# Kernel optimization log

Measured on AMD Instinct MI355X. Metric: run time of the kernel, lower is better.

## Reference

```python
import jax, jax.numpy as jnp
import numpy as np
from jax import lax

B, R, C_FEAT, HF, WF = 4, 512, 256, 50, 50
NUM_CLASSES = 91
POOL = 7
SCALE = 1.0 / 16.0
IMG_H = IMG_W = 800.0
SCORE_THRESH = 0.05
NMS_THRESH = 0.5
DETS_PER_IMG = 100
TOPK_NMS = 2048  # fixed-size candidate set for static-shape NMS
BBOX_W = np.array([10.0, 10.0, 5.0, 5.0], np.float32)
BBOX_CLIP = float(np.log(1000.0 / 16.0))
MIN_SIZE = 0.01


def setup_inputs():
    key = jax.random.key(0)
    ks = jax.random.split(key, 8)
    features = jax.random.normal(ks[0], (B, C_FEAT, HF, WF), jnp.float32)
    cxy = jax.random.uniform(ks[1], (B, R, 2), jnp.float32, 50.0, 750.0)
    wh = jax.random.uniform(ks[2], (B, R, 2), jnp.float32, 20.0, 200.0)
    proposals = jnp.concatenate([cxy - wh / 2, cxy + wh / 2], axis=-1)
    d_in = C_FEAT * POOL * POOL
    def lin(k, fi, fo):
        return jax.random.normal(k, (fi, fo), jnp.float32) / np.sqrt(fi)
    return {
        'features': features, 'proposals': proposals,
        'W1': lin(ks[3], d_in, 1024), 'b1': jnp.zeros((1024,), jnp.float32),
        'W2': lin(ks[4], 1024, 1024), 'b2': jnp.zeros((1024,), jnp.float32),
        'Wc': lin(ks[5], 1024, NUM_CLASSES), 'bc': jnp.zeros((NUM_CLASSES,), jnp.float32),
        'Wr': lin(ks[6], 1024, 4 * NUM_CLASSES), 'br': jnp.zeros((4 * NUM_CLASSES,), jnp.float32),
    }


def roi_align(features, proposals):
    # features [B,C,H,W], proposals [B,R,4] in image coords -> [B*R, C*POOL*POOL]
    featT = jnp.transpose(features, (0, 2, 3, 1))  # [B,H,W,C]
    boxes = proposals * SCALE
    x1, y1, x2, y2 = (boxes[..., i] for i in range(4))
    bh = (y2 - y1) / POOL
    bw = (x2 - x1) / POOL
    centers = jnp.arange(POOL, dtype=jnp.float32) + 0.5
    ys = y1[..., None] + centers * bh[..., None]  # [B,R,P]
    xs = x1[..., None] + centers * bw[..., None]  # [B,R,P]

    def bil(fT, ys_b, xs_b):  # per-image bilinear sampling
        yy = jnp.broadcast_to(ys_b[:, :, None], (R, POOL, POOL))
        xx = jnp.broadcast_to(xs_b[:, None, :], (R, POOL, POOL))
        y = jnp.clip(yy, 0.0, HF - 1.0)
        x = jnp.clip(xx, 0.0, WF - 1.0)
        y0 = jnp.floor(y); x0 = jnp.floor(x)
        y0i = y0.astype(jnp.int32); x0i = x0.astype(jnp.int32)
        y1i = jnp.minimum(y0i + 1, HF - 1); x1i = jnp.minimum(x0i + 1, WF - 1)
        ly = y - y0; lx = x - x0; hy = 1.0 - ly; hx = 1.0 - lx
        f00 = fT[y0i, x0i]; f01 = fT[y0i, x1i]
        f10 = fT[y1i, x0i]; f11 = fT[y1i, x1i]  # [R,P,P,C]
        out = ((hy * hx)[..., None] * f00 + (hy * lx)[..., None] * f01 +
               (ly * hx)[..., None] * f10 + (ly * lx)[..., None] * f11)
        return out  # [R,P,P,C]

    pooled = jax.vmap(bil)(featT, ys, xs)  # [B,R,P,P,C]
    pooled = jnp.transpose(pooled, (0, 1, 4, 2, 3))  # [B,R,C,P,P] (torch layout)
    return pooled.reshape(B * R, -1)


def decode_boxes(box_reg, props):
    # box_reg [N, 4*NC], props [N,4] -> [N,NC,4]
    w = props[:, 2] - props[:, 0]
    h = props[:, 3] - props[:, 1]
    cx = props[:, 0] + 0.5 * w
    cy = props[:, 1] + 0.5 * h
    d = box_reg.reshape(-1, NUM_CLASSES, 4) / jnp.asarray(BBOX_W)
    dx, dy = d[..., 0], d[..., 1]
    dw = jnp.minimum(d[..., 2], BBOX_CLIP)
    dh = jnp.minimum(d[..., 3], BBOX_CLIP)
    pcx = dx * w[:, None] + cx[:, None]
    pcy = dy * h[:, None] + cy[:, None]
    pw = jnp.exp(dw) * w[:, None]
    ph = jnp.exp(dh) * h[:, None]
    return jnp.stack([pcx - 0.5 * pw, pcy - 0.5 * ph,
                      pcx + 0.5 * pw, pcy + 0.5 * ph], axis=-1)


def box_iou(a, b):
    area_a = (a[:, 2] - a[:, 0]) * (a[:, 3] - a[:, 1])
    area_b = (b[:, 2] - b[:, 0]) * (b[:, 3] - b[:, 1])
    lt = jnp.maximum(a[:, None, :2], b[None, :, :2])
    rb = jnp.minimum(a[:, None, 2:], b[None, :, 2:])
    wh = jnp.clip(rb - lt, 0.0)
    inter = wh[..., 0] * wh[..., 1]
    return inter / (area_a[:, None] + area_b[None, :] - inter)


def post_image(boxes, scores):
    # boxes [R,NC,4], scores [R,NC] -> fixed-size top DETS_PER_IMG detections
    x1 = jnp.clip(boxes[..., 0], 0.0, IMG_W)
    y1 = jnp.clip(boxes[..., 1], 0.0, IMG_H)
    x2 = jnp.clip(boxes[..., 2], 0.0, IMG_W)
    y2 = jnp.clip(boxes[..., 3], 0.0, IMG_H)
    boxes = jnp.stack([x1, y1, x2, y2], axis=-1)
    # drop background class 0, flatten (roi, class) candidates
    boxes = boxes[:, 1:].reshape(-1, 4)            # [R*(NC-1),4]
    scores = scores[:, 1:].reshape(-1)
    labels = jnp.broadcast_to(jnp.arange(1, NUM_CLASSES, dtype=jnp.int32)[None, :],
                              (R, NUM_CLASSES - 1)).reshape(-1)
    wv = boxes[:, 2] - boxes[:, 0]
    hv = boxes[:, 3] - boxes[:, 1]
    valid = (scores > SCORE_THRESH) & (wv >= MIN_SIZE) & (hv >= MIN_SIZE)
    cand = jnp.where(valid, scores, -1.0)
    top_s, top_i = lax.top_k(cand, TOPK_NMS)       # sorted desc by score
    b_k = boxes[top_i]
    l_k = labels[top_i]
    v_k = valid[top_i]
    # batched (per-class) NMS via label offset
    off = l_k.astype(jnp.float32)[:, None] * (IMG_W + 1.0)
    iou = box_iou(b_k + off, b_k + off)            # [K,K]
    idx = jnp.arange(TOPK_NMS)

    def body(i, keep):
        sup = jnp.any((idx < i) & keep & (iou[:, i] > NMS_THRESH))
        return keep.at[i].set(keep[i] & ~sup)

    keep = lax.fori_loop(0, TOPK_NMS, body, v_k)
    fs = jnp.where(keep, top_s, -1.0)
    out_s, out_i = lax.top_k(fs, DETS_PER_IMG)
    ok = out_s > 0.0
    out_b = jnp.where(ok[:, None], b_k[out_i], 0.0)
    out_l = jnp.where(ok, l_k[out_i], 0)
    out_s = jnp.where(ok, out_s, 0.0)
    return out_b, out_s, out_l


def reference(features, proposals, W1, b1, W2, b2, Wc, bc, Wr, br):
    x = roi_align(features, proposals)               # [B*R, C*49]
    x = jax.nn.relu(x @ W1 + b1)
    x = jax.nn.relu(x @ W2 + b2)
    class_logits = x @ Wc + bc                        # [B*R, NC]
    box_regression = x @ Wr + br                      # [B*R, 4*NC]
    props_flat = proposals.reshape(-1, 4)
    pred_boxes = decode_boxes(box_regression, props_flat).reshape(B, R, NUM_CLASSES, 4)
    pred_scores = jax.nn.softmax(class_logits, axis=-1).reshape(B, R, NUM_CLASSES)
    boxes, scores, labels = jax.vmap(post_image)(pred_boxes, pred_scores)
    return boxes, scores, labels


if __name__ == '__main__':
    out = reference(**setup_inputs())
    print([o.shape for o in out])
```

## Files before the change

kernel.cpp:

```cpp
#include <hip/hip_runtime.h>
#include <stdint.h>

#define NBI 4
#define RRI 512
#define NROI 2048
#define DIN 12544
#define BBOX_CLIP_F 4.135166556742356f

typedef _Float16 half8 __attribute__((ext_vector_type(8)));
typedef float f32x16 __attribute__((ext_vector_type(16)));

#define O_AH      10240000ull
#define O_AL      61620224ull
#define O_WTH     113000448ull
#define O_WTL     138690560ull
#define OZ        164380672ull
#define WS_NEED   189546496ull

#define O_X2H     0ull
#define O_X2L     2097152ull
#define O_X1H     O_AH
#define O_X1L     (O_AH + 4194304ull)
#define O_PBOX    O_AL
#define O_KEYS    (O_AL + 2949120ull)
#define O_NMSBOX  (O_AL + 3473408ull)
#define O_OUTBOX  (O_AL + 3604480ull)
#define O_SCORE   (O_AL + 3735552ull)
#define O_LABEL   (O_AL + 3768320ull)
#define O_CNT     (O_AL + 3801088ull)
#define O_MASK    (O_AL + 3802112ull)
#define O_WHH     O_WTH
#define O_WHL     (O_WTH + 1048576ull)
#define O_BH      (O_WTH + 2097152ull)
#define O_PARTH   (O_WTH + 2101248ull)
#define O_HEADF   (O_WTH + 18878464ull)
#define O_W2TH    OZ
#define O_W2TL    (OZ + 2097152ull)
#define O_PFC2    (OZ + 4194304ull)

__global__ void k_zero_out(float* __restrict__ out) {
  int i = blockIdx.x * 256 + threadIdx.x;
  if (i < 2400) out[i] = 0.0f;
}

__global__ void k_zero2(unsigned* __restrict__ keys32, unsigned* __restrict__ cnt) {
  int i = blockIdx.x * 256 + threadIdx.x;
  if (i < 131072) keys32[i] = 0u;
  if (i < 64) cnt[i] = 0u;
}

__global__ __launch_bounds__(256) void k_transpose(const float* __restrict__ f,
                                                   float* __restrict__ ft) {
  __shared__ float s[32][33];
  int b = blockIdx.z;
  int hw0 = blockIdx.x << 5;
  int c0 = blockIdx.y << 5;
  int tx = threadIdx.x & 31, ty = threadIdx.x >> 5;
#pragma unroll
  for (int j = 0; j < 32; j += 8) {
    int hw = hw0 + tx;
    if (hw < 2500) s[ty + j][tx] = f[((size_t)b * 256 + c0 + ty + j) * 2500 + hw];
  }
  __syncthreads();
#pragma unroll
  for (int j = 0; j < 32; j += 8) {
    int hw = hw0 + ty + j;
    if (hw < 2500) ft[((size_t)b * 2500 + hw) * 256 + c0 + tx] = s[tx][ty + j];
  }
}

__global__ __launch_bounds__(256) void k_wsplit(const float* __restrict__ W,
                                                _Float16* __restrict__ Th,
                                                _Float16* __restrict__ Tl, int K, int N) {
  __shared__ float s[64][68];
  int k0 = blockIdx.x << 6, n0 = blockIdx.y << 6;
  int t = threadIdx.x;
  int r = t >> 2, c4 = (t & 3) << 4;
#pragma unroll
  for (int j = 0; j < 16; j += 4) {
    float4 v = *(const float4*)(W + (size_t)(k0 + r) * N + n0 + c4 + j);
    s[r][c4 + j] = v.x; s[r][c4 + j + 1] = v.y; s[r][c4 + j + 2] = v.z; s[r][c4 + j + 3] = v.w;
  }
  __syncthreads();
  int nr = t >> 2, kc = (t & 3) << 4;
  half8 h8[2], l8[2];
#pragma unroll
  for (int j = 0; j < 16; ++j) {
    float v = s[kc + j][nr];
    _Float16 h = (_Float16)v;
    _Float16 lo = (_Float16)((v - (float)h) * 2048.0f);
    h8[j >> 3][j & 7] = h;
    l8[j >> 3][j & 7] = lo;
  }
  size_t base = (size_t)(n0 + nr) * K + k0 + kc;
  *(half8*)(Th + base) = h8[0]; *(half8*)(Th + base + 8) = h8[1];
  *(half8*)(Tl + base) = l8[0]; *(half8*)(Tl + base + 8) = l8[1];
}

__global__ __launch_bounds__(256) void k_wsplit_heads(const float* __restrict__ Wc,
                                                      const float* __restrict__ Wr,
                                                      const float* __restrict__ bcv,
                                                      const float* __restrict__ brv,
                                                      _Float16* __restrict__ Th,
                                                      _Float16* __restrict__ Tl,
                                                      float* __restrict__ bh) {
  int n = blockIdx.x;
  int t = threadIdx.x;
  for (int k = t; k < 1024; k += 256) {
    float v = (n < 91) ? Wc[(size_t)k * 91 + n]
                       : ((n < 455) ? Wr[(size_t)k * 364 + (n - 91)] : 0.0f);
    _Float16 h = (_Float16)v;
    Th[(size_t)n * 1024 + k] = h;
    Tl[(size_t)n * 1024 + k] = (_Float16)((v - (float)h) * 2048.0f);
  }
  if (t == 0) bh[n] = (n < 91) ? bcv[n] : ((n < 455) ? brv[n - 91] : 0.0f);
}

__global__ __launch_bounds__(256) void k_roialign(const float* __restrict__ ft,
                                                  const float* __restrict__ props,
                                                  _Float16* __restrict__ Ahg,
                                                  _Float16* __restrict__ Alg) {
  __shared__ float pool[DIN];
  __shared__ float lyA[7], lxA[7];
  __shared__ int y0A[7], y1A[7], x0A[7], x1A[7];
  int roi = blockIdx.x;
  int b = roi >> 9;
  const float* p = props + (size_t)roi * 4;
  float x1s = p[0] * 0.0625f, y1s = p[1] * 0.0625f;
  float x2s = p[2] * 0.0625f, y2s = p[3] * 0.0625f;
  float bh = (y2s - y1s) / 7.0f;
  float bw = (x2s - x1s) / 7.0f;
  int t = threadIdx.x;
  if (t < 7) {
    float y = y1s + ((float)t + 0.5f) * bh;
    y = fminf(fmaxf(y, 0.0f), 49.0f);
    float y0 = floorf(y);
    int y0i = (int)y0;
    y0A[t] = y0i; y1A[t] = min(y0i + 1, 49); lyA[t] = y - y0;
  } else if (t < 14) {
    int px = t - 7;
    float x = x1s + ((float)px + 0.5f) * bw;
    x = fminf(fmaxf(x, 0.0f), 49.0f);
    float x0 = floorf(x);
    int x0i = (int)x0;
    x0A[px] = x0i; x1A[px] = min(x0i + 1, 49); lxA[px] = x - x0;
  }
  __syncthreads();
  const float* fb = ft + (size_t)b * 2500 * 256;
  int c = t;
  for (int p49 = 0; p49 < 49; ++p49) {
    int py = p49 / 7, px = p49 - py * 7;
    int y0 = y0A[py], y1 = y1A[py], x0 = x0A[px], x1 = x1A[px];
    float ly = lyA[py], lx = lxA[px], hy = 1.0f - ly, hx = 1.0f - lx;
    float f00 = fb[(y0 * 50 + x0) * 256 + c];
    float f01 = fb[(y0 * 50 + x1) * 256 + c];
    float f10 = fb[(y1 * 50 + x0) * 256 + c];
    float f11 = fb[(y1 * 50 + x1) * 256 + c];
    pool[c * 49 + p49] = (hy * hx) * f00 + (hy * lx) * f01 + (ly * hx) * f10 + (ly * lx) * f11;
  }
  __syncthreads();
  _Float16* dh = Ahg + (size_t)roi * DIN;
  _Float16* dl = Alg + (size_t)roi * DIN;
  for (int i = t; i < DIN; i += 256) {
    float v = pool[i];
    _Float16 h = (_Float16)v;
    dh[i] = h;
    dl[i] = (_Float16)((v - (float)h) * 2048.0f);
  }
}

__global__ __launch_bounds__(256, 2) void k_mfma(const _Float16* __restrict__ Ah,
                                                 const _Float16* __restrict__ Al,
                                                 const _Float16* __restrict__ Bh,
                                                 const _Float16* __restrict__ Bl,
                                                 float* __restrict__ P0,
                                                 float* __restrict__ P2,
                                                 int K, int K2, int ldc, int MN) {
  __shared__ __align__(16) _Float16 sA[2][128][32];
  __shared__ __align__(16) _Float16 sB[2][128][32];
  int gx = gridDim.x, gy = gridDim.y;
  int nwg = gx * gy * gridDim.z;
  int lin = blockIdx.x + gx * (blockIdx.y + gy * blockIdx.z);
  int cpx = nwg >> 3;
  int nl = (lin & 7) * cpx + (lin >> 3);
  int sx = __ffs(gx) - 1, sy = __ffs(gy) - 1;
  int lx = nl & (gx - 1);
  int rest = nl >> sx;
  int ly = rest & (gy - 1);
  int lz = rest >> sy;
  int m0 = ly << 7, n0 = lx << 7;
  int kb = lz * K2;
  int t = threadIdx.x;
  int w = t >> 6, l = t & 63;
  int wr = w >> 1, wc = w & 1;
  int srow = t >> 1, sh = t & 1;
  const _Float16* gAh = Ah + (size_t)(m0 + srow) * K + kb + sh * 16;
  const _Float16* gAl = Al + (size_t)(m0 + srow) * K + kb + sh * 16;
  const _Float16* gBh = Bh + (size_t)(n0 + srow) * K + kb + sh * 16;
  const _Float16* gBl = Bl + (size_t)(n0 + srow) * K + kb + sh * 16;
  int rsw = (srow >> 1) & 3;
  int wof0 = ((2 * sh) ^ rsw) << 3;
  int wof1 = ((2 * sh + 1) ^ rsw) << 3;
  f32x16 accH[2][2], accL[2][2];
#pragma unroll
  for (int i = 0; i < 2; ++i)
#pragma unroll
    for (int j = 0; j < 2; ++j)
#pragma unroll
      for (int r = 0; r < 16; ++r) { accH[i][j][r] = 0.0f; accL[i][j][r] = 0.0f; }
  half8 pAh0 = *(const half8*)gAh, pAh1 = *(const half8*)(gAh + 8);
  half8 pAl0 = *(const half8*)gAl, pAl1 = *(const half8*)(gAl + 8);
  half8 pBh0 = *(const half8*)gBh, pBh1 = *(const half8*)(gBh + 8);
  half8 pBl0 = *(const half8*)gBl, pBl1 = *(const half8*)(gBl + 8);
  int fr = l & 31, cgrp = l >> 5;
  for (int kt = 0; kt < K2; kt += 32) {
    __syncthreads();
    *(half8*)&sA[0][srow][wof0] = pAh0;
    *(half8*)&sA[0][srow][wof1] = pAh1;
    *(half8*)&sA[1][srow][wof0] = pAl0;
    *(half8*)&sA[1][srow][wof1] = pAl1;
    *(half8*)&sB[0][srow][wof0] = pBh0;
    *(half8*)&sB[0][srow][wof1] = pBh1;
    *(half8*)&sB[1][srow][wof0] = pBl0;
    *(half8*)&sB[1][srow][wof1] = pBl1;
    __syncthreads();
    if (kt + 32 < K2) {
      pAh0 = *(const half8*)(gAh + kt + 32); pAh1 = *(const half8*)(gAh + kt + 40);
      pAl0 = *(const half8*)(gAl + kt + 32); pAl1 = *(const half8*)(gAl + kt + 40);
      pBh0 = *(const half8*)(gBh + kt + 32); pBh1 = *(const half8*)(gBh + kt + 40);
      pBl0 = *(const half8*)(gBl + kt + 32); pBl1 = *(const half8*)(gBl + kt + 40);
    }
#pragma unroll
    for (int s = 0; s < 2; ++s) {
      int c2 = s * 2 + cgrp;
      half8 aH[2], aL[2], bH[2], bL[2];
#pragma unroll
      for (int mf = 0; mf < 2; ++mf) {
        int row = wr * 64 + mf * 32 + fr;
        int co = (c2 ^ ((row >> 1) & 3)) << 3;
        aH[mf] = *(const half8*)&sA[0][row][co];
        aL[mf] = *(const half8*)&sA[1][row][co];
      }
#pragma unroll
      for (int nf = 0; nf < 2; ++nf) {
        int row = wc * 64 + nf * 32 + fr;
        int co = (c2 ^ ((row >> 1) & 3)) << 3;
        bH[nf] = *(const half8*)&sB[0][row][co];
        bL[nf] = *(const half8*)&sB[1][row][co];
      }
#pragma unroll
      for (int mf = 0; mf < 2; ++mf)
#pragma unroll
        for (int nf = 0; nf < 2; ++nf) {
          accH[mf][nf] =
              __builtin_amdgcn_mfma_f32_32x32x16_f16(aH[mf], bH[nf], accH[mf][nf], 0, 0, 0);
          accL[mf][nf] =
              __builtin_amdgcn_mfma_f32_32x32x16_f16(aH[mf], bL[nf], accL[mf][nf], 0, 0, 0);
          accL[mf][nf] =
              __builtin_amdgcn_mfma_f32_32x32x16_f16(aL[mf], bH[nf], accL[mf][nf], 0, 0, 0);
        }
    }
  }
  float* Pz = (lz == 2) ? P2 : (P0 + (size_t)(lz == 3 ? 2 : lz) * MN);
  const float sc = 4.8828125e-4f;
#pragma unroll
  for (int mf = 0; mf < 2; ++mf)
#pragma unroll
    for (int nf = 0; nf < 2; ++nf) {
      int col = n0 + wc * 64 + nf * 32 + fr;
      int rbase = m0 + wr * 64 + mf * 32 + 4 * cgrp;
#pragma unroll
      for (int r = 0; r < 16; ++r) {
        int row = rbase + (r & 3) + ((r >> 2) << 3);
        Pz[(size_t)row * ldc + col] = accH[mf][nf][r] + accL[mf][nf][r] * sc;
      }
    }
}

__global__ void k_reduce_split(const float* __restrict__ P0, const float* __restrict__ P2,
                               const float* __restrict__ bias, _Float16* __restrict__ xh,
                               _Float16* __restrict__ xl, int S) {
  const int MN = 2048 * 1024;
  int i8 = blockIdx.x * 256 + threadIdx.x;
  size_t base = (size_t)i8 * 8;
  float v[8];
  {
    float4 a0 = *(const float4*)(P0 + base);
    float4 a1 = *(const float4*)(P0 + base + 4);
    float4 b0 = *(const float4*)(P0 + MN + base);
    float4 b1 = *(const float4*)(P0 + MN + base + 4);
    v[0] = a0.x + b0.x; v[1] = a0.y + b0.y; v[2] = a0.z + b0.z; v[3] = a0.w + b0.w;
    v[4] = a1.x + b1.x; v[5] = a1.y + b1.y; v[6] = a1.z + b1.z; v[7] = a1.w + b1.w;
  }
  if (S == 4) {
    float4 c0 = *(const float4*)(P2 + base);
    float4 c1 = *(const float4*)(P2 + base + 4);
    float4 d0 = *(const float4*)(P0 + 2 * (size_t)MN + base);
    float4 d1 = *(const float4*)(P0 + 2 * (size_t)MN + base + 4);
    v[0] = (v[0] + c0.x) + d0.x; v[1] = (v[1] + c0.y) + d0.y;
    v[2] = (v[2] + c0.z) + d0.z; v[3] = (v[3] + c0.w) + d0.w;
    v[4] = (v[4] + c1.x) + d1.x; v[5] = (v[5] + c1.y) + d1.y;
    v[6] = (v[6] + c1.z) + d1.z; v[7] = (v[7] + c1.w) + d1.w;
  }
  int cb = (int)(base & 1023);
  float4 b0 = *(const float4*)(bias + cb);
  float4 b1v = *(const float4*)(bias + cb + 4);
  v[0] += b0.x; v[1] += b0.y; v[2] += b0.z; v[3] += b0.w;
  v[4] += b1v.x; v[5] += b1v.y; v[6] += b1v.z; v[7] += b1v.w;
  half8 h8, l8;
#pragma unroll
  for (int j = 0; j < 8; ++j) {
    float x = fmaxf(v[j], 0.0f);
    _Float16 h = (_Float16)x;
    h8[j] = h;
    l8[j] = (_Float16)((x - (float)h) * 2048.0f);
  }
  *(half8*)(xh + base) = h8;
  *(half8*)(xl + base) = l8;
}

__global__ void k_headreduce(const float4* __restrict__ PH, const float* __restrict__ bh,
                             float4* __restrict__ head) {
  const int MN4 = 2048 * 512 / 4;
  int i = blockIdx.x * 256 + threadIdx.x;
  float4 p0 = PH[i], p1 = PH[i + MN4], p2 = PH[i + 3 * MN4], p3 = PH[i + 2 * MN4];
  const float4 b = *(const float4*)(bh + ((i & 127) << 2));
  float4 o;
  o.x = ((p0.x + p1.x) + p2.x) + p3.x + b.x;
  o.y = ((p0.y + p1.y) + p2.y) + p3.y + b.y;
  o.z = ((p0.z + p1.z) + p2.z) + p3.z + b.z;
  o.w = ((p0.w + p1.w) + p2.w) + p3.w + b.w;
  head[i] = o;
}

__global__ __launch_bounds__(256) void k_softmax_decode(const float* __restrict__ head,
                                                        const float* __restrict__ props,
                                                        float* __restrict__ pbox,
                                                        unsigned long long* __restrict__ keys,
                                                        unsigned* __restrict__ cnt) {
  int wave = threadIdx.x >> 6, lane = threadIdx.x & 63;
  int roi = (blockIdx.x << 2) + wave;
  const float* hr = head + (size_t)roi * 512;
  float l0 = hr[lane];
  float l1 = (lane < 27) ? hr[lane + 64] : -3.4e38f;
  float m = fmaxf(l0, l1);
#pragma unroll
  for (int off = 32; off; off >>= 1) m = fmaxf(m, __shfl_xor(m, off));
  float e0 = expf(l0 - m);
  float e1 = (lane < 27) ? expf(l1 - m) : 0.0f;
  float ssum = e0 + e1;
#pragma unroll
  for (int off = 32; off; off >>= 1) ssum += __shfl_xor(ssum, off);
  const float* pr = props + (size_t)roi * 4;
  float w = pr[2] - pr[0], h = pr[3] - pr[1];
  float cx = pr[0] + 0.5f * w, cy = pr[1] + 0.5f * h;
  int img = roi >> 9, rl = roi & 511;
#pragma unroll
  for (int half = 0; half < 2; ++half) {
    int c = lane + half * 64;
    float e = half ? e1 : e0;
    if (c >= 1 && c <= 90) {
      float score = e / ssum;
      const float* rg = hr + 91 + (c << 2);
      float dx = rg[0] / 10.0f, dy = rg[1] / 10.0f;
      float dw = fminf(rg[2] / 5.0f, BBOX_CLIP_F);
      float dh = fminf(rg[3] / 5.0f, BBOX_CLIP_F);
      float pcx = dx * w + cx, pcy = dy * h + cy;
      float pw = expf(dw) * w, ph = expf(dh) * h;
      float bx1 = pcx - 0.5f * pw, by1 = pcy - 0.5f * ph;
      float bx2 = pcx + 0.5f * pw, by2 = pcy + 0.5f * ph;
      bx1 = fminf(fmaxf(bx1, 0.0f), 800.0f);
      by1 = fminf(fmaxf(by1, 0.0f), 800.0f);
      bx2 = fminf(fmaxf(bx2, 0.0f), 800.0f);
      by2 = fminf(fmaxf(by2, 0.0f), 800.0f);
      float* pb = pbox + ((size_t)roi * 90 + (c - 1)) * 4;
      pb[0] = bx1; pb[1] = by1; pb[2] = bx2; pb[3] = by2;
      if (score > 0.05f && (bx2 - bx1) >= 0.01f && (by2 - by1) >= 0.01f) {
        unsigned pos = atomicAdd(cnt + img, 1u);
        unsigned idx = (unsigned)rl * 90u + (unsigned)(c - 1);
        unsigned su = __float_as_uint(score);
        su ^= (su >> 31) ? 0xFFFFFFFFu : 0x80000000u;
        keys[((size_t)img << 14) + pos] =
            ((unsigned long long)su << 32) | (unsigned long long)(0xFFFFFFFFu - idx);
      }
    }
  }
}

__global__ void k_sort(unsigned long long* __restrict__ keys, const unsigned* __restrict__ cnt) {
  extern __shared__ unsigned long long s[];
  int img = blockIdx.x, tid = threadIdx.x;
  unsigned long long* kb = keys + ((size_t)img << 14);
  unsigned n = cnt[img];
  unsigned np = 2048; while (np < n && np < 16384) np <<= 1;
  if (np <= 8192) {
    for (unsigned i = tid; i < np; i += 1024) s[i] = kb[i];
    __syncthreads();
    for (unsigned k = 2; k <= np; k <<= 1) {
      for (unsigned j = k >> 1; j; j >>= 1) {
        for (unsigned x = tid; x < (np >> 1); x += 1024) {
          unsigned i = ((x & ~(j - 1)) << 1) | (x & (j - 1));
          unsigned l = i | j;
          bool up = ((i & k) == 0);
          unsigned long long a = s[i], b = s[l];
          if ((a > b) == up) { s[i] = b; s[l] = a; }
        }
        __syncthreads();
      }
    }
    for (unsigned i = tid; i < np; i += 1024) kb[i] = s[i];
  } else {
    for (int ch = 0; ch < 2; ++ch) {
      unsigned base = (unsigned)ch << 13;
      for (unsigned i = tid; i < 8192; i += 1024) s[i] = kb[base + i];
      __syncthreads();
      for (unsigned k = 2; k <= 8192; k <<= 1) {
        for (unsigned j = k >> 1; j; j >>= 1) {
          for (unsigned x = tid; x < 4096; x += 1024) {
            unsigned i = ((x & ~(j - 1)) << 1) | (x & (j - 1));
            unsigned l = i | j;
            bool up = (((base + i) & k) == 0);
            unsigned long long a = s[i], b = s[l];
            if ((a > b) == up) { s[i] = b; s[l] = a; }
          }
          __syncthreads();
        }
      }
      for (unsigned i = tid; i < 8192; i += 1024) kb[base + i] = s[i];
      __syncthreads();
    }
    for (unsigned x = tid; x < 8192; x += 1024) {
      unsigned long long a = kb[x], b = kb[x + 8192];
      if (a > b) { kb[x] = b; kb[x + 8192] = a; }
    }
    __syncthreads();
    for (int ch = 0; ch < 2; ++ch) {
      unsigned base = (unsigned)ch << 13;
      for (unsigned i = tid; i < 8192; i += 1024) s[i] = kb[base + i];
      __syncthreads();
      for (unsigned j = 4096; j; j >>= 1) {
        for (unsigned x = tid; x < 4096; x += 1024) {
          unsigned i = ((x & ~(j - 1)) << 1) | (x & (j - 1));
          unsigned l = i | j;
          unsigned long long a = s[i], b = s[l];
          if (a > b) { s[i] = b; s[l] = a; }
        }
        __syncthreads();
      }
      for (unsigned i = tid; i < 8192; i += 1024) kb[base + i] = s[i];
      __syncthreads();
    }
  }
}

__global__ void k_gather(const unsigned long long* __restrict__ keys,
                         const unsigned* __restrict__ cnt, const float* __restrict__ pbox,
                         float4* __restrict__ nmsbox, float4* __restrict__ outbox,
                         float* __restrict__ score, float* __restrict__ label) {
  int g = blockIdx.x * 256 + threadIdx.x;
  int img = g >> 11, slot = g & 2047;
  unsigned n = cnt[img];
  unsigned neff = n > 2048u ? 2048u : n;
  unsigned np = 2048; while (np < n && np < 16384) np <<= 1;
  float4 bo = make_float4(0, 0, 0, 0), bx = make_float4(0, 0, 0, 0);
  float sc = -1.0f, lb = 0.0f;
  if ((unsigned)slot < neff) {
    unsigned long long key = keys[((size_t)img << 14) + (np - 1 - slot)];
    unsigned su = (unsigned)(key >> 32);
    su = (su & 0x80000000u) ? (su ^ 0x80000000u) : ~su;
    sc = __uint_as_float(su);
    unsigned idx = 0xFFFFFFFFu - (unsigned)(key & 0xFFFFFFFFull);
    unsigned rl = idx / 90u, c = idx - rl * 90u;
    const float* pb = pbox + ((size_t)((img << 9) + rl) * 90 + c) * 4;
    bx = *(const float4*)pb;
    float off = (float)(c + 1) * 801.0f;
    bo = make_float4(bx.x + off, bx.y + off, bx.z + off, bx.w + off);
    lb = (float)(c + 1);
  }
  nmsbox[g] = bo; outbox[g] = bx; score[g] = sc; label[g] = lb;
}

__global__ __launch_bounds__(256) void k_mask(const float* __restrict__ nmsbox,
                                              unsigned* __restrict__ mask) {
  __shared__ float bx[2048 * 4];
  int img = blockIdx.x >> 9;
  int i0 = (blockIdx.x & 511) << 2;
  const float4* src = (const float4*)(nmsbox + (size_t)img * 2048 * 4);
  for (int q = threadIdx.x; q < 2048; q += 256) ((float4*)bx)[q] = src[q];
  __syncthreads();
  int w = threadIdx.x & 63, ir = threadIdx.x >> 6;
  int i = i0 + ir;
  float ax1 = bx[i * 4], ay1 = bx[i * 4 + 1], ax2 = bx[i * 4 + 2], ay2 = bx[i * 4 + 3];
  float areaA = (ax2 - ax1) * (ay2 - ay1);
  unsigned bits = 0;
  for (int jj = 0; jj < 32; ++jj) {
    int j2 = (jj + w) & 31;
    int j = (w << 5) + j2;
    float b1 = bx[j * 4], b2 = bx[j * 4 + 1], b3 = bx[j * 4 + 2], b4 = bx[j * 4 + 3];
    float areaB = (b3 - b1) * (b4 - b2);
    float lx = fmaxf(ax1, b1), lyv = fmaxf(ay1, b2);
    float rx = fminf(ax2, b3), ry = fminf(ay2, b4);
    float iw = fmaxf(rx - lx, 0.0f), ih = fmaxf(ry - lyv, 0.0f);
    float inter = iw * ih;
    float iou = inter / (areaA + areaB - inter);
    if (iou > 0.5f) bits |= (1u << j2);
  }
  mask[((size_t)img * 2048 + i) * 64 + w] = bits;
}

__global__ void k_scan(const unsigned* __restrict__ mask, const unsigned* __restrict__ cnt,
                       const float* __restrict__ outbox, const float* __restrict__ score,
                       const float* __restrict__ label, float* __restrict__ dout) {
  int img = blockIdx.x, lane = threadIdx.x;
  unsigned n = cnt[img];
  unsigned neff = n > 2048u ? 2048u : n;
  unsigned base = (unsigned)lane * 32u;
  unsigned rem;
  if (base + 32u <= neff) rem = 0u;
  else if (base >= neff) rem = 0xFFFFFFFFu;
  else rem = ~((1u << (neff - base)) - 1u);
  const unsigned* mrow = mask + (size_t)img * 2048 * 64;
  unsigned row = (neff > 0) ? mrow[lane] : 0u;
  int outc = 0;
  for (int i = 0; i < (int)neff; ++i) {
    unsigned nextrow = (i + 1 < (int)neff) ? mrow[(size_t)(i + 1) * 64 + lane] : 0u;
    unsigned wrd = __shfl(rem, i >> 5);
    bool kept = ((wrd >> (i & 31)) & 1u) == 0u;
    if (kept) {
      rem |= row;
      if (lane < 4)
        dout[(size_t)(img * 100 + outc) * 4 + lane] = outbox[((size_t)img * 2048 + i) * 4 + lane];
      if (lane == 0) {
        dout[1600 + img * 100 + outc] = score[img * 2048 + i];
        dout[2000 + img * 100 + outc] = label[img * 2048 + i];
      }
      ++outc;
      if (outc >= 100) break;
    }
    row = nextrow;
  }
}

extern "C" void kernel_launch(void* const* d_in, const int* in_sizes, int n_in,
                              void* d_out, int out_size, void* d_ws, size_t ws_size,
                              hipStream_t stream) {
  if (ws_size < WS_NEED) return;

  const float* features  = (const float*)d_in[0];
  const float* proposals = (const float*)d_in[1];
  const float* W1 = (const float*)d_in[2];
  const float* b1 = (const float*)d_in[3];
  const float* W2 = (const float*)d_in[4];
  const float* b2 = (const float*)d_in[5];
  const float* Wc = (const float*)d_in[6];
  const float* bc = (const float*)d_in[7];
  const float* Wr = (const float*)d_in[8];
  const float* br = (const float*)d_in[9];
  float* out = (float*)d_out;
  char* ws = (char*)d_ws;

  float* featT = (float*)(ws + 0);
  _Float16* Ahg = (_Float16*)(ws + O_AH);
  _Float16* Alg = (_Float16*)(ws + O_AL);
  _Float16* Wth = (_Float16*)(ws + O_WTH);
  _Float16* Wtl = (_Float16*)(ws + O_WTL);
  float* partZ = (float*)(ws + OZ);
  float* partF = (float*)(ws + 0);
  _Float16* x1h = (_Float16*)(ws + O_X1H);
  _Float16* x1l = (_Float16*)(ws + O_X1L);
  _Float16* W2th = (_Float16*)(ws + O_W2TH);
  _Float16* W2tl = (_Float16*)(ws + O_W2TL);
  float* partC = (float*)(ws + O_PFC2);
  _Float16* x2h = (_Float16*)(ws + O_X2H);
  _Float16* x2l = (_Float16*)(ws + O_X2L);
  _Float16* whh = (_Float16*)(ws + O_WHH);
  _Float16* whl = (_Float16*)(ws + O_WHL);
  float* bhv   = (float*)(ws + O_BH);
  float* partH = (float*)(ws + O_PARTH);
  float* partH2 = (float*)(ws + O_PARTH + 3ull * 4194304ull);
  float* head  = (float*)(ws + O_HEADF);
  float* pbox  = (float*)(ws + O_PBOX);
  unsigned long long* keys = (unsigned long long*)(ws + O_KEYS);
  float* nmsbox = (float*)(ws + O_NMSBOX);
  float* outbox = (float*)(ws + O_OUTBOX);
  float* scorea = (float*)(ws + O_SCORE);
  float* labela = (float*)(ws + O_LABEL);
  unsigned* cnt = (unsigned*)(ws + O_CNT);
  unsigned* maska = (unsigned*)(ws + O_MASK);

  k_zero_out<<<10, 256, 0, stream>>>(out);
  k_transpose<<<dim3(79, 8, 4), 256, 0, stream>>>(features, featT);
  k_wsplit<<<dim3(196, 16), 256, 0, stream>>>(W1, Wth, Wtl, 12544, 1024);
  k_roialign<<<2048, 256, 0, stream>>>(featT, proposals, Ahg, Alg);
  k_mfma<<<dim3(8, 16, 4), 256, 0, stream>>>(Ahg, Alg, Wth, Wtl, partZ, partF,
                                             12544, 3136, 1024, 2048 * 1024);
  k_reduce_split<<<1024, 256, 0, stream>>>(partZ, partF, b1, x1h, x1l, 4);
  k_wsplit<<<dim3(16, 16), 256, 0, stream>>>(W2, W2th, W2tl, 1024, 1024);
  k_wsplit_heads<<<512, 256, 0, stream>>>(Wc, Wr, bc, br, whh, whl, bhv);
  k_mfma<<<dim3(8, 16, 2), 256, 0, stream>>>(x1h, x1l, W2th, W2tl, partC, partC,
                                             1024, 512, 1024, 2048 * 1024);
  k_reduce_split<<<1024, 256, 0, stream>>>(partC, partC, b2, x2h, x2l, 2);
  k_mfma<<<dim3(4, 16, 4), 256, 0, stream>>>(x2h, x2l, whh, whl, partH, partH2,
                                             1024, 256, 512, 2048 * 512);
  k_headreduce<<<1024, 256, 0, stream>>>((const float4*)partH, bhv, (float4*)head);
  k_zero2<<<512, 256, 0, stream>>>((unsigned*)keys, cnt);
  k_softmax_decode<<<512, 256, 0, stream>>>(head, proposals, pbox, keys, cnt);
  k_sort<<<4, 1024, 65536, stream>>>(keys, cnt);
  k_gather<<<32, 256, 0, stream>>>(keys, cnt, pbox, (float4*)nmsbox, (float4*)outbox,
                                   scorea, labela);
  k_mask<<<2048, 256, 0, stream>>>(nmsbox, maska);
  k_scan<<<4, 64, 0, stream>>>(maska, cnt, outbox, scorea, labela, out);
}
```

Before: 395.6 us.

## Load B fragments directly from global into registers and double-buffer A in LDS

The MFMA GEMM kernel no longer stages the B (weight) tile in shared memory. Each wave now loads its own B fragments straight from global memory into registers, prefetching the next k-slice while the current one computes. The A tile goes into a double-buffered LDS array, so each k-step needs one barrier instead of two. The aim is less LDS traffic and fewer barriers, at the cost of uncoalesced per-lane global reads of B (16 bytes per row) and more register pressure.

```diff
diff --git a/kernel.cpp b/kernel.cpp
--- a/kernel.cpp
+++ b/kernel.cpp
@@ -176,8 +176,7 @@
                                                  float* __restrict__ P0,
                                                  float* __restrict__ P2,
                                                  int K, int K2, int ldc, int MN) {
-  __shared__ __align__(16) _Float16 sA[2][128][32];
-  __shared__ __align__(16) _Float16 sB[2][128][32];
+  __shared__ __align__(16) _Float16 sA[2][2][128][32];
   int gx = gridDim.x, gy = gridDim.y;
   int nwg = gx * gy * gridDim.z;
   int lin = blockIdx.x + gx * (blockIdx.y + gy * blockIdx.z);
@@ -193,14 +192,17 @@
   int t = threadIdx.x;
   int w = t >> 6, l = t & 63;
   int wr = w >> 1, wc = w & 1;
+  int fr = l & 31, cgrp = l >> 5;
   int srow = t >> 1, sh = t & 1;
   const _Float16* gAh = Ah + (size_t)(m0 + srow) * K + kb + sh * 16;
   const _Float16* gAl = Al + (size_t)(m0 + srow) * K + kb + sh * 16;
-  const _Float16* gBh = Bh + (size_t)(n0 + srow) * K + kb + sh * 16;
-  const _Float16* gBl = Bl + (size_t)(n0 + srow) * K + kb + sh * 16;
   int rsw = (srow >> 1) & 3;
   int wof0 = ((2 * sh) ^ rsw) << 3;
   int wof1 = ((2 * sh + 1) ^ rsw) << 3;
+  const _Float16* pBh0 = Bh + (size_t)(n0 + wc * 64 + fr) * K + kb + cgrp * 8;
+  const _Float16* pBh1 = Bh + (size_t)(n0 + wc * 64 + 32 + fr) * K + kb + cgrp * 8;
+  const _Float16* pBl0 = Bl + (size_t)(n0 + wc * 64 + fr) * K + kb + cgrp * 8;
+  const _Float16* pBl1 = Bl + (size_t)(n0 + wc * 64 + 32 + fr) * K + kb + cgrp * 8;
   f32x16 accH[2][2], accL[2][2];
 #pragma unroll
   for (int i = 0; i < 2; ++i)
@@ -210,55 +212,70 @@
       for (int r = 0; r < 16; ++r) { accH[i][j][r] = 0.0f; accL[i][j][r] = 0.0f; }
   half8 pAh0 = *(const half8*)gAh, pAh1 = *(const half8*)(gAh + 8);
   half8 pAl0 = *(const half8*)gAl, pAl1 = *(const half8*)(gAl + 8);
-  half8 pBh0 = *(const half8*)gBh, pBh1 = *(const half8*)(gBh + 8);
-  half8 pBl0 = *(const half8*)gBl, pBl1 = *(const half8*)(gBl + 8);
-  int fr = l & 31, cgrp = l >> 5;
+  *(half8*)&sA[0][0][srow][wof0] = pAh0;
+  *(half8*)&sA[0][0][srow][wof1] = pAh1;
+  *(half8*)&sA[0][1][srow][wof0] = pAl0;
+  *(half8*)&sA[0][1][srow][wof1] = pAl1;
+  half8 cbh0 = *(const half8*)pBh0;
+  half8 cbh1 = *(const half8*)pBh1;
+  half8 cbl0 = *(const half8*)pBl0;
+  half8 cbl1 = *(const half8*)pBl1;
+  __syncthreads();
   for (int kt = 0; kt < K2; kt += 32) {
-    __syncthreads();
-    *(half8*)&sA[0][srow][wof0] = pAh0;
-    *(half8*)&sA[0][srow][wof1] = pAh1;
-    *(half8*)&sA[1][srow][wof0] = pAl0;
-    *(half8*)&sA[1][srow][wof1] = pAl1;
-    *(half8*)&sB[0][srow][wof0] = pBh0;
-    *(half8*)&sB[0][srow][wof1] = pBh1;
-    *(half8*)&sB[1][srow][wof0] = pBl0;
-    *(half8*)&sB[1][srow][wof1] = pBl1;
-    __syncthreads();
-    if (kt + 32 < K2) {
+    int buf = (kt >> 5) & 1;
+    bool more = (kt + 32) < K2;
+    if (more) {
       pAh0 = *(const half8*)(gAh + kt + 32); pAh1 = *(const half8*)(gAh + kt + 40);
       pAl0 = *(const half8*)(gAl + kt + 32); pAl1 = *(const half8*)(gAl + kt + 40);
-      pBh0 = *(const half8*)(gBh + kt + 32); pBh1 = *(const half8*)(gBh + kt + 40);
-      pBl0 = *(const half8*)(gBl + kt + 32); pBl1 = *(const half8*)(gBl + kt + 40);
-    }
-#pragma unroll
-    for (int s = 0; s < 2; ++s) {
-      int c2 = s * 2 + cgrp;
-      half8 aH[2], aL[2], bH[2], bL[2];
+    }
+    half8 nbh0 = *(const half8*)(pBh0 + kt + 16);
+    half8 nbh1 = *(const half8*)(pBh1 + kt + 16);
+    half8 nbl0 = *(const half8*)(pBl0 + kt + 16);
+    half8 nbl1 = *(const half8*)(pBl1 + kt + 16);
+    {
+      int c2 = cgrp;
 #pragma unroll
       for (int mf = 0; mf < 2; ++mf) {
         int row = wr * 64 + mf * 32 + fr;
         int co = (c2 ^ ((row >> 1) & 3)) << 3;
-        aH[mf] = *(const half8*)&sA[0][row][co];
-        aL[mf] = *(const half8*)&sA[1][row][co];
-      }
-#pragma unroll
-      for (int nf = 0; nf < 2; ++nf) {
-        int row = wc * 64 + nf * 32 + fr;
+        half8 aH = *(const half8*)&sA[buf][0][row][co];
+        half8 aL = *(const half8*)&sA[buf][1][row][co];
+        accH[mf][0] = __builtin_amdgcn_mfma_f32_32x32x16_f16(aH, cbh0, accH[mf][0], 0, 0, 0);
+        accL[mf][0] = __builtin_amdgcn_mfma_f32_32x32x16_f16(aH, cbl0, accL[mf][0], 0, 0, 0);
+        accL[mf][0] = __builtin_amdgcn_mfma_f32_32x32x16_f16(aL, cbh0, accL[mf][0], 0, 0, 0);
+        accH[mf][1] = __builtin_amdgcn_mfma_f32_32x32x16_f16(aH, cbh1, accH[mf][1], 0, 0, 0);
+        accL[mf][1] = __builtin_amdgcn_mfma_f32_32x32x16_f16(aH, cbl1, accL[mf][1], 0, 0, 0);
+        accL[mf][1] = __builtin_amdgcn_mfma_f32_32x32x16_f16(aL, cbh1, accL[mf][1], 0, 0, 0);
+      }
+    }
+    if (more) {
+      cbh0 = *(const half8*)(pBh0 + kt + 32);
+      cbh1 = *(const half8*)(pBh1 + kt + 32);
+      cbl0 = *(const half8*)(pBl0 + kt + 32);
+      cbl1 = *(const half8*)(pBl1 + kt + 32);
+    }
+    {
+      int c2 = 2 + cgrp;
+#pragma unroll
+      for (int mf = 0; mf < 2; ++mf) {
+        int row = wr * 64 + mf * 32 + fr;
         int co = (c2 ^ ((row >> 1) & 3)) << 3;
-        bH[nf] = *(const half8*)&sB[0][row][co];
-        bL[nf] = *(const half8*)&sB[1][row][co];
-      }
-#pragma unroll
-      for (int mf = 0; mf < 2; ++mf)
-#pragma unroll
-        for (int nf = 0; nf < 2; ++nf) {
-          accH[mf][nf] =
-              __builtin_amdgcn_mfma_f32_32x32x16_f16(aH[mf], bH[nf], accH[mf][nf], 0, 0, 0);
-          accL[mf][nf] =
-              __builtin_amdgcn_mfma_f32_32x32x16_f16(aH[mf], bL[nf], accL[mf][nf], 0, 0, 0);
-          accL[mf][nf] =
-              __builtin_amdgcn_mfma_f32_32x32x16_f16(aL[mf], bH[nf], accL[mf][nf], 0, 0, 0);
-        }
+        half8 aH = *(const half8*)&sA[buf][0][row][co];
+        half8 aL = *(const half8*)&sA[buf][1][row][co];
+        accH[mf][0] = __builtin_amdgcn_mfma_f32_32x32x16_f16(aH, nbh0, accH[mf][0], 0, 0, 0);
+        accL[mf][0] = __builtin_amdgcn_mfma_f32_32x32x16_f16(aH, nbl0, accL[mf][0], 0, 0, 0);
+        accL[mf][0] = __builtin_amdgcn_mfma_f32_32x32x16_f16(aL, nbh0, accL[mf][0], 0, 0, 0);
+        accH[mf][1] = __builtin_amdgcn_mfma_f32_32x32x16_f16(aH, nbh1, accH[mf][1], 0, 0, 0);
+        accL[mf][1] = __builtin_amdgcn_mfma_f32_32x32x16_f16(aH, nbl1, accL[mf][1], 0, 0, 0);
+        accL[mf][1] = __builtin_amdgcn_mfma_f32_32x32x16_f16(aL, nbh1, accL[mf][1], 0, 0, 0);
+      }
+    }
+    if (more) {
+      *(half8*)&sA[buf ^ 1][0][srow][wof0] = pAh0;
+      *(half8*)&sA[buf ^ 1][0][srow][wof1] = pAh1;
+      *(half8*)&sA[buf ^ 1][1][srow][wof0] = pAl0;
+      *(half8*)&sA[buf ^ 1][1][srow][wof1] = pAl1;
+      __syncthreads();
     }
   }
   float* Pz = (lz == 2) ? P2 : (P0 + (size_t)(lz == 3 ? 2 : lz) * MN);
```

Result: slower. 487.9 us (+23.3%).

## Double-buffer MFMA GEMM shared tiles and switch to fragment-major LDS layout

Applied to the files above, without the earlier changes.

Splits the shared-memory A/B tiles into two ping-pong buffers. The next k-tile is written to LDS while MFMAs consume the current one, and global loads run two tiles ahead. This drops one of the two barriers per k-step. It also replaces the XOR-swizzled row layout with a fragment-major half8 layout, so each lane reads contiguous 16-byte vectors without index arithmetic. LDS use doubles to 64 KB per block, which may limit occupancy under the 2-blocks-per-CU launch bound.

```diff
diff --git a/kernel.cpp b/kernel.cpp
--- a/kernel.cpp
+++ b/kernel.cpp
@@ -176,8 +176,8 @@
                                                  float* __restrict__ P0,
                                                  float* __restrict__ P2,
                                                  int K, int K2, int ldc, int MN) {
-  __shared__ __align__(16) _Float16 sA[2][128][32];
-  __shared__ __align__(16) _Float16 sB[2][128][32];
+  __shared__ __align__(16) half8 sA[2][2][512];
+  __shared__ __align__(16) half8 sB[2][2][512];
   int gx = gridDim.x, gy = gridDim.y;
   int nwg = gx * gy * gridDim.z;
   int lin = blockIdx.x + gx * (blockIdx.y + gy * blockIdx.z);
@@ -193,14 +193,16 @@
   int t = threadIdx.x;
   int w = t >> 6, l = t & 63;
   int wr = w >> 1, wc = w & 1;
-  int srow = t >> 1, sh = t & 1;
-  const _Float16* gAh = Ah + (size_t)(m0 + srow) * K + kb + sh * 16;
-  const _Float16* gAl = Al + (size_t)(m0 + srow) * K + kb + sh * 16;
-  const _Float16* gBh = Bh + (size_t)(n0 + srow) * K + kb + sh * 16;
-  const _Float16* gBl = Bl + (size_t)(n0 + srow) * K + kb + sh * 16;
-  int rsw = (srow >> 1) & 3;
-  int wof0 = ((2 * sh) ^ rsw) << 3;
-  int wof1 = ((2 * sh + 1) ^ rsw) << 3;
+  int fr = l & 31, cgrp = l >> 5;
+  int sr = t >> 1, sh = t & 1;
+  const _Float16* gAh = Ah + (size_t)(m0 + sr) * K + kb + sh * 16;
+  const _Float16* gAl = Al + (size_t)(m0 + sr) * K + kb + sh * 16;
+  const _Float16* gBh = Bh + (size_t)(n0 + sr) * K + kb + sh * 16;
+  const _Float16* gBl = Bl + (size_t)(n0 + sr) * K + kb + sh * 16;
+  int ws0 = ((sr >> 5) * 4 + 2 * sh) * 32 + (sr & 31);
+  int ws1 = ws0 + 32;
+  int sa0 = wr * 256 + cgrp * 32 + fr;
+  int sb0 = wc * 256 + cgrp * 32 + fr;
   f32x16 accH[2][2], accL[2][2];
 #pragma unroll
   for (int i = 0; i < 2; ++i)
@@ -208,45 +210,50 @@
     for (int j = 0; j < 2; ++j)
 #pragma unroll
       for (int r = 0; r < 16; ++r) { accH[i][j][r] = 0.0f; accL[i][j][r] = 0.0f; }
-  half8 pAh0 = *(const half8*)gAh, pAh1 = *(const half8*)(gAh + 8);
-  half8 pAl0 = *(const half8*)gAl, pAl1 = *(const half8*)(gAl + 8);
-  half8 pBh0 = *(const half8*)gBh, pBh1 = *(const half8*)(gBh + 8);
-  half8 pBl0 = *(const half8*)gBl, pBl1 = *(const half8*)(gBl + 8);
-  int fr = l & 31, cgrp = l >> 5;
+  half8 rAh0 = *(const half8*)gAh, rAh1 = *(const half8*)(gAh + 8);
+  half8 rAl0 = *(const half8*)gAl, rAl1 = *(const half8*)(gAl + 8);
+  half8 rBh0 = *(const half8*)gBh, rBh1 = *(const half8*)(gBh + 8);
+  half8 rBl0 = *(const half8*)gBl, rBl1 = *(const half8*)(gBl + 8);
+  sA[0][0][ws0] = rAh0; sA[0][0][ws1] = rAh1;
+  sA[0][1][ws0] = rAl0; sA[0][1][ws1] = rAl1;
+  sB[0][0][ws0] = rBh0; sB[0][0][ws1] = rBh1;
+  sB[0][1][ws0] = rBl0; sB[0][1][ws1] = rBl1;
+  if (32 < K2) {
+    rAh0 = *(const half8*)(gAh + 32); rAh1 = *(const half8*)(gAh + 40);
+    rAl0 = *(const half8*)(gAl + 32); rAl1 = *(const half8*)(gAl + 40);
+    rBh0 = *(const half8*)(gBh + 32); rBh1 = *(const half8*)(gBh + 40);
+    rBl0 = *(const half8*)(gBl + 32); rBl1 = *(const half8*)(gBl + 40);
+  }
+  __syncthreads();
   for (int kt = 0; kt < K2; kt += 32) {
-    __syncthreads();
-    *(half8*)&sA[0][srow][wof0] = pAh0;
-    *(half8*)&sA[0][srow][wof1] = pAh1;
-    *(half8*)&sA[1][srow][wof0] = pAl0;
-    *(half8*)&sA[1][srow][wof1] = pAl1;
-    *(half8*)&sB[0][srow][wof0] = pBh0;
-    *(half8*)&sB[0][srow][wof1] = pBh1;
-    *(half8*)&sB[1][srow][wof0] = pBl0;
-    *(half8*)&sB[1][srow][wof1] = pBl1;
-    __syncthreads();
-    if (kt + 32 < K2) {
-      pAh0 = *(const half8*)(gAh + kt + 32); pAh1 = *(const half8*)(gAh + kt + 40);
-      pAl0 = *(const half8*)(gAl + kt + 32); pAl1 = *(const half8*)(gAl + kt + 40);
-      pBh0 = *(const half8*)(gBh + kt + 32); pBh1 = *(const half8*)(gBh + kt + 40);
-      pBl0 = *(const half8*)(gBl + kt + 32); pBl1 = *(const half8*)(gBl + kt + 40);
+    int buf = (kt >> 5) & 1;
+    bool more = (kt + 32) < K2;
+    if (more) {
+      sA[buf ^ 1][0][ws0] = rAh0; sA[buf ^ 1][0][ws1] = rAh1;
+      sA[buf ^ 1][1][ws0] = rAl0; sA[buf ^ 1][1][ws1] = rAl1;
+      sB[buf ^ 1][0][ws0] = rBh0; sB[buf ^ 1][0][ws1] = rBh1;
+      sB[buf ^ 1][1][ws0] = rBl0; sB[buf ^ 1][1][ws1] = rBl1;
+    }
+    if ((kt + 64) < K2) {
+      rAh0 = *(const half8*)(gAh + kt + 64); rAh1 = *(const half8*)(gAh + kt + 72);
+      rAl0 = *(const half8*)(gAl + kt + 64); rAl1 = *(const half8*)(gAl + kt + 72);
+      rBh0 = *(const half8*)(gBh + kt + 64); rBh1 = *(const half8*)(gBh + kt + 72);
+      rBl0 = *(const half8*)(gBl + kt + 64); rBl1 = *(const half8*)(gBl + kt + 72);
     }
 #pragma unroll
     for (int s = 0; s < 2; ++s) {
-      int c2 = s * 2 + cgrp;
       half8 aH[2], aL[2], bH[2], bL[2];
 #pragma unroll
       for (int mf = 0; mf < 2; ++mf) {
-        int row = wr * 64 + mf * 32 + fr;
-        int co = (c2 ^ ((row >> 1) & 3)) << 3;
-        aH[mf] = *(const half8*)&sA[0][row][co];
-        aL[mf] = *(const half8*)&sA[1][row][co];
+        int sa = sa0 + mf * 128 + s * 64;
+        aH[mf] = sA[buf][0][sa];
+        aL[mf] = sA[buf][1][sa];
       }
 #pragma unroll
       for (int nf = 0; nf < 2; ++nf) {
-        int row = wc * 64 + nf * 32 + fr;
-        int co = (c2 ^ ((row >> 1) & 3)) << 3;
-        bH[nf] = *(const half8*)&sB[0][row][co];
-        bL[nf] = *(const half8*)&sB[1][row][co];
+        int sb = sb0 + nf * 128 + s * 64;
+        bH[nf] = sB[buf][0][sb];
+        bL[nf] = sB[buf][1][sb];
       }
 #pragma unroll
       for (int mf = 0; mf < 2; ++mf)
@@ -260,6 +267,7 @@
               __builtin_amdgcn_mfma_f32_32x32x16_f16(aL[mf], bH[nf], accL[mf][nf], 0, 0, 0);
         }
     }
+    if (more) __syncthreads();
   }
   float* Pz = (lz == 2) ? P2 : (P0 + (size_t)(lz == 3 ? 2 : lz) * MN);
   const float sc = 4.8828125e-4f;
```

New measurement: 383.8 us. -3.0%, faster.
